# Kernel tuning notes

Measured on AMD Instinct MI355X. Metric: run time of the kernel, lower is better.

## Reference

```python
import jax, jax.numpy as jnp
import numpy as np

IOU_THRESHOLD = 0.5

def cxcywh_to_xyxy(b):
    cx, cy, w, h = jnp.split(b, 4, axis=-1)
    return jnp.concatenate([cx - 0.5 * w, cy - 0.5 * h, cx + 0.5 * w, cy + 0.5 * h], axis=-1)

def batched_giou(p_xyxy, t_xyxy):
    # p_xyxy: [B, N, 4], t_xyxy: [B, T, 4] -> giou: [B, N, T]
    p = p_xyxy[:, :, None, :]  # [B, N, 1, 4]
    t = t_xyxy[:, None, :, :]  # [B, 1, T, 4]
    area_p = (p_xyxy[..., 2] - p_xyxy[..., 0]) * (p_xyxy[..., 3] - p_xyxy[..., 1])  # [B, N]
    area_t = (t_xyxy[..., 2] - t_xyxy[..., 0]) * (t_xyxy[..., 3] - t_xyxy[..., 1])  # [B, T]
    lt = jnp.maximum(p[..., :2], t[..., :2])
    rb = jnp.minimum(p[..., 2:], t[..., 2:])
    wh = jnp.clip(rb - lt, 0.0)
    inter = wh[..., 0] * wh[..., 1]  # [B, N, T]
    union = area_p[:, :, None] + area_t[:, None, :] - inter
    iou = inter / union
    # enclosing box
    lt_e = jnp.minimum(p[..., :2], t[..., :2])
    rb_e = jnp.maximum(p[..., 2:], t[..., 2:])
    wh_e = jnp.clip(rb_e - lt_e, 0.0)
    area_e = wh_e[..., 0] * wh_e[..., 1]
    return iou - (area_e - union) / area_e

def setup_inputs() -> dict:
    key = jax.random.key(0)
    k1, k2 = jax.random.split(key)
    B, N, T = 128, 900, 300
    pred_boxes = jax.random.uniform(k1, (B, N, 4), dtype=jnp.float32)
    target_boxes = jax.random.uniform(k2, (B, T, 4), dtype=jnp.float32)
    target_mask = jnp.ones((B, T), dtype=bool)
    return {"pred_boxes": pred_boxes, "target_boxes": target_boxes, "target_mask": target_mask}

def reference(pred_boxes, target_boxes, target_mask):
    # pred_boxes: [B, N, 4] cxcywh; target_boxes: [B, T, 4] cxcywh (padded)
    p_xyxy = cxcywh_to_xyxy(pred_boxes)
    t_xyxy = cxcywh_to_xyxy(target_boxes)
    giou = batched_giou(p_xyxy, t_xyxy)  # [B, N, T]
    max_iou = jnp.max(giou, axis=1)      # [B, T] best GIoU per target
    pred_idx = jnp.argmax(giou, axis=1)  # [B, T] matched query per target
    valid = target_mask & (max_iou >= IOU_THRESHOLD)  # [B, T] match kept
    return pred_idx, valid, max_iou
```

## Files before the change

### kernel.cpp

```cpp
#include <hip/hip_runtime.h>


#define BB 128
#define NN 900
#define TT 300
#define TCHUNK 64
#define TBLOCKS 5
#define NWAVES 8
#define MARGIN 2e-5f

__device__ __forceinline__ float giou_exact(float4 pb, float4 tb) {
#pragma clang fp contract(off)
    float px0 = pb.x - 0.5f * pb.z, py0 = pb.y - 0.5f * pb.w;
    float px1 = pb.x + 0.5f * pb.z, py1 = pb.y + 0.5f * pb.w;
    float tx0 = tb.x - 0.5f * tb.z, ty0 = tb.y - 0.5f * tb.w;
    float tx1 = tb.x + 0.5f * tb.z, ty1 = tb.y + 0.5f * tb.w;
    float pa = (px1 - px0) * (py1 - py0);
    float ta = (tx1 - tx0) * (ty1 - ty0);
    float w  = fmaxf(fminf(px1, tx1) - fmaxf(px0, tx0), 0.f);
    float h  = fmaxf(fminf(py1, ty1) - fmaxf(py0, ty0), 0.f);
    float inter = w * h;
    float uni   = pa + ta - inter;
    float iou   = inter / uni;
    float ew = fmaxf(fmaxf(px1, tx1) - fminf(px0, tx0), 0.f);
    float eh = fmaxf(fmaxf(py1, ty1) - fminf(py0, ty0), 0.f);
    float ea = ew * eh;
    return iou - (ea - uni) / ea;
}

__global__ __launch_bounds__(512) void matcher_kernel(
    const float* __restrict__ pred,
    const float* __restrict__ tgt,
    const unsigned char* __restrict__ mask,
    float* __restrict__ out)
{
    __shared__ float4 sp[NN];
    __shared__ float  rbv[NWAVES * TCHUNK], rsv[NWAVES * TCHUNK];
    __shared__ int    riv[NWAVES * TCHUNK];
    __shared__ int    sflag[TCHUNK];
    __shared__ int    scount;

    const int tc  = blockIdx.x % TBLOCKS;
    const int b   = blockIdx.x / TBLOCKS;
    const int tid = threadIdx.x;
    const int l   = tid & 63;
    const int wv  = tid >> 6;
    const int t   = tc * TCHUNK + l;

    if (tid == 0) scount = 0;

    for (int i = tid; i < NN; i += 512) {
        const float4 pb = ((const float4*)pred)[b * NN + i];
        float4 q;
        q.x = pb.x - 0.5f * pb.z;
        q.y = pb.y - 0.5f * pb.w;
        q.z = pb.x + 0.5f * pb.z;
        q.w = pb.y + 0.5f * pb.w;
        sp[i] = q;
    }

    float tx0 = 0.f, ty0 = 0.f, tx1 = 0.f, ty1 = 0.f, ta = 0.f, wtx = 0.f, wty = 0.f;
    if (t < TT) {
        const float4 tb = ((const float4*)tgt)[b * TT + t];
        tx0 = tb.x - 0.5f * tb.z;
        ty0 = tb.y - 0.5f * tb.w;
        tx1 = tb.x + 0.5f * tb.z;
        ty1 = tb.y + 0.5f * tb.w;
        wtx = tx1 - tx0;
        wty = ty1 - ty0;
        ta  = wtx * wty;
    }
    __syncthreads();

    const int start = wv * 112 + min(wv, 4);
    const int len   = 112 + (wv < 4 ? 1 : 0);

    float best = -INFINITY, sec = -INFINITY;
    int   bidxl = 0;
    #pragma unroll 4
    for (int k = 0; k < len; ++k) {
        const float4 q = sp[start + k];
        const float wpx = q.z - q.x;
        const float wpy = q.w - q.y;
        const float pa  = wpx * wpy;

        const float ew = fmaxf(q.z, tx1) - fminf(q.x, tx0);
        const float eh = fmaxf(q.w, ty1) - fminf(q.y, ty0);
        const float w  = fmaxf((wpx + wtx) - ew, 0.f);
        const float h  = fmaxf((wpy + wty) - eh, 0.f);
        const float inter = w * h;
        const float ea    = ew * eh;
        const float uni   = (pa + ta) - inter;
        const float den   = uni * ea;
        const float num = fmaf(inter, ea, fmaf(uni, uni, -den));
        const float g   = num * __builtin_amdgcn_rcpf(den);

        sec = __builtin_amdgcn_fmed3f(g, best, sec);
        if (g > best) bidxl = k;
        best = fmaxf(best, g);
    }

    rbv[wv * TCHUNK + l] = best;
    rsv[wv * TCHUNK + l] = sec;
    riv[wv * TCHUNK + l] = start + bidxl;
    __syncthreads();

    if (tid < TCHUNK && t < TT) {
        float bb = -INFINITY, ss = -INFINITY;
        int   bi = 0;
        #pragma unroll
        for (int s = 0; s < NWAVES; ++s) {
            const float ob = rbv[s * TCHUNK + tid];
            const float os = rsv[s * TCHUNK + tid];
            const int   oi = riv[s * TCHUNK + tid];
            ss = fmaxf(fminf(bb, ob), fmaxf(ss, os));
            if (ob > bb) { bb = ob; bi = oi; }
        }
        const int bt = b * TT + t;
        if (bb - ss > MARGIN) {
            const float4 pb = ((const float4*)pred)[b * NN + bi];
            const float4 tb = ((const float4*)tgt)[bt];
            const float g = giou_exact(pb, tb);
            const bool valid = (mask[bt] != 0) && (g >= 0.5f);
            out[bt]               = (float)bi;
            out[BB * TT + bt]     = valid ? 1.f : 0.f;
            out[2 * BB * TT + bt] = g;
        } else {
            const int pos = atomicAdd(&scount, 1);
            sflag[pos] = t;
        }
    }
    __syncthreads();

    const int cnt = scount;
    for (int f = wv; f < cnt; f += NWAVES) {
        const int ft  = sflag[f];
        const int fbt = b * TT + ft;
        const float4 tb = ((const float4*)tgt)[fbt];

        float bx = -INFINITY;
        int   bi = NN;
        for (int n = l; n < NN; n += 64) {
            const float4 pb = ((const float4*)pred)[b * NN + n];
            const float g = giou_exact(pb, tb);
            if (g > bx) { bx = g; bi = n; }
        }
        for (int off = 32; off >= 1; off >>= 1) {
            const float ob = __shfl_xor(bx, off);
            const int   oi = __shfl_xor(bi, off);
            if (ob > bx || (ob == bx && oi < bi)) { bx = ob; bi = oi; }
        }
        if (l == 0) {
            const bool valid = (mask[fbt] != 0) && (bx >= 0.5f);
            out[fbt]               = (float)bi;
            out[BB * TT + fbt]     = valid ? 1.f : 0.f;
            out[2 * BB * TT + fbt] = bx;
        }
    }
}

extern "C" void kernel_launch(void* const* d_in, const int* in_sizes, int n_in,
                              void* d_out, int out_size, void* d_ws, size_t ws_size,
                              hipStream_t stream) {
    const float* pred = (const float*)d_in[0];
    const float* tgt  = (const float*)d_in[1];
    const unsigned char* mask = (const unsigned char*)d_in[2];
    float* out = (float*)d_out;

    matcher_kernel<<<dim3(BB * TBLOCKS), dim3(512), 0, stream>>>(
        pred, tgt, mask, out);
}
```

Measured before the change: 95.61 us.

## Split prediction scan across two blocks and finish in a second kernel

The single fused kernel becomes two kernels. The first scans half of the predictions per block with 256 threads and writes partial best, second-best and index to workspace. The second merges the two partials, recomputes the exact GIoU, and runs the full fallback scan for ambiguous targets. This doubles the block count to raise occupancy and parallelism. In exchange it adds a kernel launch, global round-trips for the partial results, and a fallback loop with less parallelism per block.

Result: no change. 95.60 us (-0.0%).

```diff
diff --git a/kernel.cpp b/kernel.cpp
--- a/kernel.cpp
+++ b/kernel.cpp
@@ -6,7 +6,8 @@
 #define TT 300
 #define TCHUNK 64
 #define TBLOCKS 5
-#define NWAVES 8
+#define NSPLIT 2
+#define NPB 450
 #define MARGIN 2e-5f
 
 __device__ __forceinline__ float giou_exact(float4 pb, float4 tb) {
@@ -28,29 +29,27 @@
     return iou - (ea - uni) / ea;
 }
 
-__global__ __launch_bounds__(512) void matcher_kernel(
+__global__ __launch_bounds__(256) void matcher_scan_kernel(
     const float* __restrict__ pred,
     const float* __restrict__ tgt,
-    const unsigned char* __restrict__ mask,
-    float* __restrict__ out)
+    float* __restrict__ pbest,
+    float* __restrict__ psec,
+    int*   __restrict__ pidx)
 {
-    __shared__ float4 sp[NN];
-    __shared__ float  rbv[NWAVES * TCHUNK], rsv[NWAVES * TCHUNK];
-    __shared__ int    riv[NWAVES * TCHUNK];
-    __shared__ int    sflag[TCHUNK];
-    __shared__ int    scount;
-
-    const int tc  = blockIdx.x % TBLOCKS;
-    const int b   = blockIdx.x / TBLOCKS;
+    __shared__ float4 sp[NPB];
+    __shared__ float  rbv[4 * TCHUNK], rsv[4 * TCHUNK];
+    __shared__ int    riv[4 * TCHUNK];
+
+    const int ns  = blockIdx.x & 1;
+    const int tc  = (blockIdx.x >> 1) % TBLOCKS;
+    const int b   = blockIdx.x / (NSPLIT * TBLOCKS);
     const int tid = threadIdx.x;
     const int l   = tid & 63;
     const int wv  = tid >> 6;
     const int t   = tc * TCHUNK + l;
 
-    if (tid == 0) scount = 0;
-
-    for (int i = tid; i < NN; i += 512) {
-        const float4 pb = ((const float4*)pred)[b * NN + i];
+    for (int i = tid; i < NPB; i += 256) {
+        const float4 pb = ((const float4*)pred)[b * NN + ns * NPB + i];
         float4 q;
         q.x = pb.x - 0.5f * pb.z;
         q.y = pb.y - 0.5f * pb.w;
@@ -72,8 +71,8 @@
     }
     __syncthreads();
 
-    const int start = wv * 112 + min(wv, 4);
-    const int len   = 112 + (wv < 4 ? 1 : 0);
+    const int start = wv * 112 + min(wv, 2);
+    const int len   = 112 + (wv < 2 ? 1 : 0);
 
     float best = -INFINITY, sec = -INFINITY;
     int   bidxl = 0;
@@ -105,42 +104,78 @@
     riv[wv * TCHUNK + l] = start + bidxl;
     __syncthreads();
 
-    if (tid < TCHUNK && t < TT) {
-        float bb = -INFINITY, ss = -INFINITY;
-        int   bi = 0;
+    if (wv == 0 && t < TT) {
+        float bb = best, ss = sec;
+        int   bi = start + bidxl;
         #pragma unroll
-        for (int s = 0; s < NWAVES; ++s) {
-            const float ob = rbv[s * TCHUNK + tid];
-            const float os = rsv[s * TCHUNK + tid];
-            const int   oi = riv[s * TCHUNK + tid];
+        for (int s = 1; s < 4; ++s) {
+            const float ob = rbv[s * TCHUNK + l];
+            const float os = rsv[s * TCHUNK + l];
+            const int   oi = riv[s * TCHUNK + l];
             ss = fmaxf(fminf(bb, ob), fmaxf(ss, os));
             if (ob > bb) { bb = ob; bi = oi; }
         }
         const int bt = b * TT + t;
-        if (bb - ss > MARGIN) {
-            const float4 pb = ((const float4*)pred)[b * NN + bi];
-            const float4 tb = ((const float4*)tgt)[bt];
-            const float g = giou_exact(pb, tb);
-            const bool valid = (mask[bt] != 0) && (g >= 0.5f);
-            out[bt]               = (float)bi;
-            out[BB * TT + bt]     = valid ? 1.f : 0.f;
-            out[2 * BB * TT + bt] = g;
-        } else {
-            const int pos = atomicAdd(&scount, 1);
-            sflag[pos] = t;
-        }
-    }
-    __syncthreads();
-
-    const int cnt = scount;
-    for (int f = wv; f < cnt; f += NWAVES) {
-        const int ft  = sflag[f];
-        const int fbt = b * TT + ft;
+        pbest[ns * BB * TT + bt] = bb;
+        psec [ns * BB * TT + bt] = ss;
+        pidx [ns * BB * TT + bt] = ns * NPB + bi;
+    }
+}
+
+__global__ __launch_bounds__(256) void matcher_finish_kernel(
+    const float* __restrict__ pbest,
+    const float* __restrict__ psec,
+    const int*   __restrict__ pidx,
+    const float* __restrict__ pred,
+    const float* __restrict__ tgt,
+    const unsigned char* __restrict__ mask,
+    float* __restrict__ out)
+{
+    __shared__ int sflag[256];
+    __shared__ int scount;
+
+    const int tid = threadIdx.x;
+    const int bt  = blockIdx.x * 256 + tid;
+    if (tid == 0) scount = 0;
+    __syncthreads();
+
+    float best = -INFINITY, second = -INFINITY;
+    int   bidx = 0;
+    #pragma unroll
+    for (int s = 0; s < NSPLIT; ++s) {
+        const float ob = pbest[s * BB * TT + bt];
+        const float os = psec [s * BB * TT + bt];
+        const int   oi = pidx [s * BB * TT + bt];
+        second = fmaxf(fminf(best, ob), fmaxf(second, os));
+        if (ob > best) { best = ob; bidx = oi; }
+    }
+
+    if (best - second > MARGIN) {
+        const int b = bt / TT;
+        const float4 pb = ((const float4*)pred)[b * NN + bidx];
+        const float4 tb = ((const float4*)tgt)[bt];
+        const float g = giou_exact(pb, tb);
+        const bool valid = (mask[bt] != 0) && (g >= 0.5f);
+        out[bt]               = (float)bidx;
+        out[BB * TT + bt]     = valid ? 1.f : 0.f;
+        out[2 * BB * TT + bt] = g;
+    } else {
+        const int pos = atomicAdd(&scount, 1);
+        sflag[pos] = tid;
+    }
+    __syncthreads();
+
+    const int cnt  = scount;
+    const int lane = tid & 63;
+    const int wv   = tid >> 6;
+    for (int f = wv; f < cnt; f += 4) {
+        const int fbt = blockIdx.x * 256 + sflag[f];
+        const int b   = fbt / TT;
         const float4 tb = ((const float4*)tgt)[fbt];
 
         float bx = -INFINITY;
         int   bi = NN;
-        for (int n = l; n < NN; n += 64) {
+        for (int n = lane; n < NN; n += 64) {
             const float4 pb = ((const float4*)pred)[b * NN + n];
             const float g = giou_exact(pb, tb);
             if (g > bx) { bx = g; bi = n; }
@@ -150,7 +185,7 @@
             const int   oi = __shfl_xor(bi, off);
             if (ob > bx || (ob == bx && oi < bi)) { bx = ob; bi = oi; }
         }
-        if (l == 0) {
+        if (lane == 0) {
             const bool valid = (mask[fbt] != 0) && (bx >= 0.5f);
             out[fbt]               = (float)bi;
             out[BB * TT + fbt]     = valid ? 1.f : 0.f;
@@ -167,6 +202,14 @@
     const unsigned char* mask = (const unsigned char*)d_in[2];
     float* out = (float*)d_out;
 
-    matcher_kernel<<<dim3(BB * TBLOCKS), dim3(512), 0, stream>>>(
-        pred, tgt, mask, out);
-}
+    const size_t seg = (size_t)NSPLIT * BB * TT * 4;
+    char* ws = (char*)d_ws;
+    float* pbest = (float*)ws;
+    float* psec  = (float*)(ws + seg);
+    int*   pidx  = (int*)  (ws + 2 * seg);
+
+    matcher_scan_kernel<<<dim3(BB * TBLOCKS * NSPLIT), dim3(256), 0, stream>>>(
+        pred, tgt, pbest, psec, pidx);
+    matcher_finish_kernel<<<dim3(BB * TT / 256), dim3(256), 0, stream>>>(
+        pbest, psec, pidx, pred, tgt, mask, out);
+}
```
